# Performance work log

Measured on AMD Instinct MI355X. Metric: run time of the kernel, lower is better.

The kernel has to match this reference:

```python
import jax, jax.numpy as jnp
import numpy as np

N, E, F = 50000, 400000, 128
H0, C0 = 1, 128   # layer 0: heads=1, out=128 (concat=False -> mean over heads)
H1, C1 = 4, 64    # layer 1: heads=4, out=64
EPS_BN = 1e-5
NEG_SLOPE = 0.2


def setup_inputs() -> dict:
    key = jax.random.key(0)
    ks = jax.random.split(key, 12)

    def w(k, shape, fan_in):
        return jax.random.normal(k, shape, jnp.float32) / np.float32(np.sqrt(fan_in))

    return {
        "emb": jax.random.normal(ks[0], (N, F), jnp.float32),
        "edge_weight": jax.random.uniform(ks[1], (E,), jnp.float32),
        # GATv2Conv layer 0 params (lin_l, lin_r, lin_edge, att, out bias)
        "Wl0": w(ks[2], (F, H0 * C0), F), "bl0": jnp.zeros((H0 * C0,), jnp.float32),
        "Wr0": w(ks[3], (F, H0 * C0), F), "br0": jnp.zeros((H0 * C0,), jnp.float32),
        "We0": w(ks[4], (1, H0 * C0), 1), "att0": w(ks[5], (H0, C0), C0),
        "b0": jnp.zeros((C0,), jnp.float32),
        "g0": jnp.ones((C0,), jnp.float32), "be0": jnp.zeros((C0,), jnp.float32),
        # GATv2Conv layer 1 params
        "Wl1": w(ks[6], (C0, H1 * C1), C0), "bl1": jnp.zeros((H1 * C1,), jnp.float32),
        "Wr1": w(ks[7], (C0, H1 * C1), C0), "br1": jnp.zeros((H1 * C1,), jnp.float32),
        "We1": w(ks[8], (1, H1 * C1), 1), "att1": w(ks[9], (H1, C1), C1),
        "b1": jnp.zeros((C1,), jnp.float32),
        "g1": jnp.ones((C1,), jnp.float32), "be1": jnp.zeros((C1,), jnp.float32),
        "edge_index": jax.random.randint(ks[10], (2, E), 0, N, jnp.int32),
    }


def gatv2(x, src, dst, ea, Wl, bl, Wr, br, We, att, b, H, C):
    """PyG GATv2Conv, edge_dim=1, concat=False (mean over heads), eval dropout."""
    n = x.shape[0]
    xl = (x @ Wl + bl).reshape(n, H, C)
    xr = (x @ Wr + br).reshape(n, H, C)
    ef = (ea[:, None] @ We).reshape(-1, H, C)           # [Et,H,C] edge embedding
    m = jax.nn.leaky_relu(xl[src] + xr[dst] + ef, NEG_SLOPE)  # [Et,H,C]
    alpha = jnp.einsum('ehc,hc->eh', m, att)            # attention logits
    amax = jax.ops.segment_max(alpha, dst, num_segments=n)
    ex = jnp.exp(alpha - amax[dst])
    den = jax.ops.segment_sum(ex, dst, num_segments=n)
    a = ex / (den[dst] + 1e-16)                          # segment softmax (PyG eps)
    out = jax.ops.segment_sum(a[:, :, None] * xl[src], dst, num_segments=n)
    return out.mean(axis=1) + b                          # concat=False -> head mean


def batchnorm(x, g, be):
    mu = x.mean(0)
    v = x.var(0)  # biased variance, as torch BN uses for normalization
    return g * (x - mu) * jax.lax.rsqrt(v + EPS_BN) + be


def _forward(emb, edge_weight, Wl0, bl0, Wr0, br0, We0, att0, b0, g0, be0,
             Wl1, bl1, Wr1, br1, We1, att1, b1, g1, be1, edge_index):
    loop = jnp.arange(N, dtype=edge_index.dtype)
    src = jnp.concatenate([edge_index[0], loop])
    dst = jnp.concatenate([edge_index[1], loop])
    # add_self_loops with fill_value='mean' for edge_attr
    ea = jnp.concatenate([edge_weight, jnp.full((N,), edge_weight.mean(), edge_weight.dtype)])
    # NOTE: zip(layer_stack, batchnorm_stack) truncates -> only first 2 of 3 GAT
    # layers execute, each followed by BN + ELU (+ identity dropout, p=0).
    h = gatv2(emb, src, dst, ea, Wl0, bl0, Wr0, br0, We0, att0, b0, H0, C0)
    h = jax.nn.elu(batchnorm(h, g0, be0))
    h = gatv2(h, src, dst, ea, Wl1, bl1, Wr1, br1, We1, att1, b1, H1, C1)
    h = jax.nn.elu(batchnorm(h, g1, be1))
    return h


def reference(emb, edge_weight, Wl0, bl0, Wr0, br0, We0, att0, b0, g0, be0,
              Wl1, bl1, Wr1, br1, We1, att1, b1, g1, be1, edge_index):
    return _forward(emb, edge_weight, Wl0, bl0, Wr0, br0, We0, att0, b0, g0, be0,
                    Wl1, bl1, Wr1, br1, We1, att1, b1, g1, be1, edge_index)
```

## Files before the change

kernel.cpp:

```cpp
#include <hip/hip_runtime.h>
#include <cstdint>
#include <cstddef>
#include <type_traits>

using f32x4 = __attribute__((ext_vector_type(4))) float;
using s16x8 = __attribute__((ext_vector_type(8))) short;

__device__ __forceinline__ ushort f2bf(float x) {
    uint32_t u = __builtin_bit_cast(uint32_t, x);
    u += 0x7fffu + ((u >> 16) & 1u);
    return (ushort)(u >> 16);
}
__device__ __forceinline__ float bflo(uint32_t u) { return __builtin_bit_cast(float, u << 16); }
__device__ __forceinline__ float bfhi(uint32_t u) { return __builtin_bit_cast(float, u & 0xffff0000u); }

__device__ __forceinline__ void dec8(uint4 g, float* x) {
    x[0] = bflo(g.x); x[1] = bfhi(g.x); x[2] = bflo(g.y); x[3] = bfhi(g.y);
    x[4] = bflo(g.z); x[5] = bfhi(g.z); x[6] = bflo(g.w); x[7] = bfhi(g.w);
}

#define GLOAD_LDS16(g, l)                                                                  \
    __builtin_amdgcn_global_load_lds((const __attribute__((address_space(1))) void*)(g),  \
                                     (__attribute__((address_space(3))) void*)(l), 16, 0, 0)

__global__ __launch_bounds__(256) void degree_ew_wt(const int* __restrict__ ei,
                                                    const float* __restrict__ ew,
                                                    int* __restrict__ deg,
                                                    float* __restrict__ partials,
                                                    int E, int N, int NBE,
                                                    const float* __restrict__ Wl0,
                                                    const float* __restrict__ Wr0,
                                                    ushort* __restrict__ WT0,
                                                    const float* __restrict__ Wl1,
                                                    const float* __restrict__ Wr1,
                                                    ushort* __restrict__ WT1) {
    __shared__ float red[256];
    int bid = blockIdx.x;
    int t = threadIdx.x;
    if (bid < NBE) {
        int e = bid * 256 + t;
        float s = (e < E) ? ew[e] : 0.f;
        red[t] = s; __syncthreads();
        for (int o = 128; o; o >>= 1) { if (t < o) red[t] += red[t + o]; __syncthreads(); }
        if (t == 0) partials[bid] = red[0];
        if (e < E + N) {
            int d = (e < E) ? ei[E + e] : (e - E);
            atomicAdd(&deg[d], 1);
        }
        return;
    }
    int j = (bid - NBE) * 256 + t;
    if (j < 128 * 256) {
        int k = j >> 8, c = j & 255;
        float v = (c < 128) ? Wl0[k * 128 + c] : Wr0[k * 128 + (c - 128)];
        WT0[(size_t)c * 128 + k] = f2bf(v);
        return;
    }
    j -= 128 * 256;
    if (j < 128 * 512) {
        int k = j >> 9, c = j & 511;
        float v = (c < 256) ? Wl1[k * 256 + c] : Wr1[k * 256 + (c - 256)];
        WT1[(size_t)c * 128 + k] = f2bf(v);
    }
}

__global__ void scan_partial(const int* __restrict__ deg, int n, int* __restrict__ bsum) {
    __shared__ int lds[256];
    int t = threadIdx.x;
    int base = blockIdx.x * 1024 + t * 4;
    int s = 0;
#pragma unroll
    for (int j = 0; j < 4; ++j) if (base + j < n) s += deg[base + j];
    lds[t] = s; __syncthreads();
    for (int o = 128; o; o >>= 1) { if (t < o) lds[t] += lds[t + o]; __syncthreads(); }
    if (t == 0) bsum[blockIdx.x] = lds[0];
}

__global__ void scan_block(const int* __restrict__ bsum, int nb, int* __restrict__ boff,
                           int* __restrict__ row_start, int n, int total,
                           const float* __restrict__ partials, int nbp, int E,
                           float* __restrict__ stats) {
    __shared__ int lds[256];
    __shared__ float fred[256];
    int t = threadIdx.x;
    int v = (t < nb) ? bsum[t] : 0;
    lds[t] = v; __syncthreads();
    for (int o = 1; o < 256; o <<= 1) {
        int y = (t >= o) ? lds[t - o] : 0;
        __syncthreads();
        lds[t] += y;
        __syncthreads();
    }
    if (t < nb) boff[t] = lds[t] - v;
    if (t == 0) row_start[n] = total;
    stats[t] = 0.f; stats[256 + t] = 0.f;
    float fs = 0.f;
    for (int j = t; j < nbp; j += 256) fs += partials[j];
    fred[t] = fs; __syncthreads();
    for (int o = 128; o; o >>= 1) { if (t < o) fred[t] += fred[t + o]; __syncthreads(); }
    if (t == 0) stats[0] = fred[0] / (float)E;
}

__global__ void scan_final(const int* __restrict__ deg, int n, const int* __restrict__ boff,
                           int* __restrict__ row_start, int* __restrict__ cursor) {
    __shared__ int lds[256];
    int t = threadIdx.x;
    int base = blockIdx.x * 1024 + t * 4;
    int d[4], loc[4], s = 0;
#pragma unroll
    for (int j = 0; j < 4; ++j) d[j] = (base + j < n) ? deg[base + j] : 0;
#pragma unroll
    for (int j = 0; j < 4; ++j) { loc[j] = s; s += d[j]; }
    lds[t] = s; __syncthreads();
    for (int o = 1; o < 256; o <<= 1) {
        int y = (t >= o) ? lds[t - o] : 0;
        __syncthreads();
        lds[t] += y;
        __syncthreads();
    }
    int texcl = lds[t] - s + boff[blockIdx.x];
#pragma unroll
    for (int j = 0; j < 4; ++j)
        if (base + j < n) { row_start[base + j] = texcl + loc[j]; cursor[base + j] = 0; }
}

__global__ void scatter_kernel(const int* __restrict__ ei, const float* __restrict__ ew,
                               const float* __restrict__ ew_mean, const int* __restrict__ row_start,
                               int* __restrict__ cursor, int* __restrict__ csr_src,
                               float* __restrict__ csr_ea, int E, int N) {
    int e = blockIdx.x * blockDim.x + threadIdx.x;
    if (e >= E + N) return;
    int s, d; float w;
    if (e < E) { s = ei[e]; d = ei[E + e]; w = ew[e]; }
    else       { s = d = e - E;            w = ew_mean[0]; }
    int pos = row_start[d] + atomicAdd(&cursor[d], 1);
    csr_src[pos] = s;
    csr_ea[pos] = w;
}

template <int MODE>
__global__ __launch_bounds__(512) void mfma_linear3(const void* __restrict__ Xv,
                                                    const ushort* __restrict__ WT,
                                                    const float* __restrict__ bnsums,
                                                    const float* __restrict__ gamma,
                                                    const float* __restrict__ beta,
                                                    const float* __restrict__ bl,
                                                    const float* __restrict__ br,
                                                    ushort* __restrict__ xl,
                                                    ushort* __restrict__ xr,
                                                    int n, int HALF) {
    constexpr int LW = (MODE == 1) ? 2 : 1;
    __shared__ ushort sB[128 * 128];
    __shared__ ushort sA[128 * 128];
    const int tid = threadIdx.x;
    const int c0 = blockIdx.x * 128;
    const int ntiles = (n + 127) >> 7;

    {
        const ushort* src = WT + (size_t)c0 * 128;
#pragma unroll
        for (int it = 0; it < 4; ++it) {
            int f = tid + it * 512;
            int row = f >> 4, ch = f & 15;
            const ushort* g = src + (size_t)row * 128 + ((ch ^ (row & 7)) << 3);
            ushort* lp = sB + (((size_t)it * 512 + (tid & ~63)) << 3);
            GLOAD_LDS16(g, lp);
        }
    }

    const int myc = (tid & 15) * 8;
    const int row0 = tid >> 4;
    const int swc = (tid & 15) ^ (row0 & 7);
    float Af[8], Bf[8];
    if constexpr (MODE == 2) {
        float invn = 1.f / (float)n;
#pragma unroll
        for (int j = 0; j < 8; ++j) {
            float mu = bnsums[myc + j] * invn;
            float var = bnsums[128 + myc + j] * invn - mu * mu;
            float rs = rsqrtf(var + 1e-5f);
            Af[j] = gamma[myc + j] * rs;
            Bf[j] = beta[myc + j] - mu * Af[j];
        }
    }

    uint4 rA[4][LW];
    auto loadA = [&](int rt) {
        int r0 = rt << 7;
#pragma unroll
        for (int it = 0; it < 4; ++it) {
            int gr = r0 + row0 + it * 32; gr = gr < n ? gr : n - 1;
            if constexpr (MODE == 1) {
                const float* src = (const float*)Xv + (size_t)gr * 128 + myc;
                rA[it][0] = *(const uint4*)src;
                rA[it][1] = *(const uint4*)(src + 4);
            } else {
                rA[it][0] = *(const uint4*)((const ushort*)Xv + (size_t)gr * 128 + myc);
            }
        }
    };
    auto writeA = [&]() {
#pragma unroll
        for (int it = 0; it < 4; ++it) {
            uint4 o;
            if constexpr (MODE == 0) {
                o = rA[it][0];
            } else if constexpr (MODE == 1) {
                float x[8] = {
                    __builtin_bit_cast(float, rA[it][0].x), __builtin_bit_cast(float, rA[it][0].y),
                    __builtin_bit_cast(float, rA[it][0].z), __builtin_bit_cast(float, rA[it][0].w),
                    __builtin_bit_cast(float, rA[it][1].x), __builtin_bit_cast(float, rA[it][1].y),
                    __builtin_bit_cast(float, rA[it][1].z), __builtin_bit_cast(float, rA[it][1].w)};
                ushort h[8];
#pragma unroll
                for (int j = 0; j < 8; ++j) h[j] = f2bf(x[j]);
                o.x = h[0] | ((uint32_t)h[1] << 16); o.y = h[2] | ((uint32_t)h[3] << 16);
                o.z = h[4] | ((uint32_t)h[5] << 16); o.w = h[6] | ((uint32_t)h[7] << 16);
            } else {
                float x[8]; dec8(rA[it][0], x);
                ushort h[8];
#pragma unroll
                for (int j = 0; j < 8; ++j) {
                    float v = fmaf(x[j], Af[j], Bf[j]);
                    v = v > 0.f ? v : __expf(v) - 1.f;
                    h[j] = f2bf(v);
                }
                o.x = h[0] | ((uint32_t)h[1] << 16); o.y = h[2] | ((uint32_t)h[3] << 16);
                o.z = h[4] | ((uint32_t)h[5] << 16); o.w = h[6] | ((uint32_t)h[7] << 16);
            }
            *(uint4*)&sA[(row0 + it * 32) * 128 + swc * 8] = o;
        }
    };

    const int w = tid >> 6, l = tid & 63, lr = l & 15, lg = l >> 4;
    const bool left = c0 < HALF;
    const float* bias = left ? bl : br;
    ushort* dst = left ? xl : xr;
    const int cb = left ? c0 : c0 - HALF;
    float bv[8];
#pragma unroll
    for (int tn = 0; tn < 8; ++tn) bv[tn] = bias[cb + tn * 16 + lr];
    const int arow = w * 16 + lr;

    int rt = blockIdx.y;
    if (rt >= ntiles) return;
    loadA(rt);
    writeA();
    __syncthreads();

    while (true) {
        int nx = rt + gridDim.y;
        if (nx < ntiles) loadA(nx);

        f32x4 acc[8] = {};
#pragma unroll
        for (int kk = 0; kk < 4; ++kk) {
            int ach = (kk * 4 + lg) ^ (arow & 7);
            s16x8 a = *(const s16x8*)&sA[arow * 128 + (ach << 3)];
#pragma unroll
            for (int tn = 0; tn < 8; ++tn) {
                int brow = tn * 16 + lr;
                int bch = (kk * 4 + lg) ^ (brow & 7);
                s16x8 b = *(const s16x8*)&sB[brow * 128 + (bch << 3)];
                acc[tn] = __builtin_amdgcn_mfma_f32_16x16x32_bf16(a, b, acc[tn], 0, 0, 0);
            }
        }
        int rbase = (rt << 7) + w * 16 + lg * 4;
#pragma unroll
        for (int tn = 0; tn < 8; ++tn) {
            int colh = cb + tn * 16 + lr;
#pragma unroll
            for (int r = 0; r < 4; ++r) {
                int row = rbase + r;
                if (row < n) dst[(size_t)row * HALF + colh] = f2bf(acc[tn][r] + bv[tn]);
            }
        }
        if (nx >= ntiles) break;
        __syncthreads();
        writeA();
        __syncthreads();
        rt = nx;
    }
}

template <int H, int C, int LPN>
__global__ __launch_bounds__(256, 6) void gat_agg(const ushort* __restrict__ xl,
                                                  const ushort* __restrict__ xr,
                                                  const int* __restrict__ row_start,
                                                  const int* __restrict__ csr_src,
                                                  const float* __restrict__ csr_ea,
                                                  const float* __restrict__ We,
                                                  const float* __restrict__ att,
                                                  const float* __restrict__ bias,
                                                  ushort* __restrict__ out, int n) {
    constexpr int HC = H * C;
    constexpr int VPL = HC / LPN;
    constexpr int REDW = LPN / H;
    constexpr int NPW = 64 / LPN;
    static_assert(VPL == 8, "");

    const int wid = threadIdx.x >> 6;
    const int lane = threadIdx.x & 63;
    const int sl = lane & (LPN - 1);
    const int sub = lane / LPN;
    const int v = (blockIdx.x * 4 + wid) * NPW + sub;
    const bool valid = v < n;
    const int vv = valid ? v : n - 1;

    const int base = sl * VPL;
    const int e0 = row_start[vv];
    const int e1 = row_start[vv + 1];
    const ushort* xlb = xl + base;

    uint4 gF; float wF;
    {
        int s = csr_src[e0];
        wF = csr_ea[e0];
        gF = *(const uint4*)&xlb[(size_t)s * HC];
    }
    uint4 gA, gB; float wA, wB;
    {
        int ea = e0 + 1 < e1 ? e0 + 1 : e0;
        int eb = e0 + 2 < e1 ? e0 + 2 : e0;
        int sa = csr_src[ea]; wA = csr_ea[ea];
        int sb = csr_src[eb]; wB = csr_ea[eb];
        gA = *(const uint4*)&xlb[(size_t)sa * HC];
        gB = *(const uint4*)&xlb[(size_t)sb * HC];
    }

    float xrv[8], wE[8], attv[8];
    dec8(*(const uint4*)&xr[(size_t)vv * HC + base], xrv);
#pragma unroll
    for (int j = 0; j < 8; j += 4) {
        float4 a = *(const float4*)&We[base + j];
        wE[j] = a.x; wE[j + 1] = a.y; wE[j + 2] = a.z; wE[j + 3] = a.w;
        float4 b = *(const float4*)&att[base + j];
        attv[j] = b.x; attv[j + 1] = b.y; attv[j + 2] = b.z; attv[j + 3] = b.w;
    }

    float m, den, acc[8];
    {
        float xf[8];
        dec8(gF, xf);
        float t1 = 0.f, t2 = 0.f;
#pragma unroll
        for (int j = 0; j < 8; ++j) {
            float u = xf[j] + fmaf(wF, wE[j], xrv[j]);
            t1 = fmaf(u, attv[j], t1);
            t2 = fmaf(__builtin_fabsf(u), attv[j], t2);
        }
        float p = fmaf(0.6f, t1, 0.4f * t2);
#pragma unroll
        for (int o = REDW >> 1; o; o >>= 1) p += __shfl_xor(p, o, 64);
        m = p; den = 1.f;
#pragma unroll
        for (int j = 0; j < 8; ++j) acc[j] = xf[j];
    }

    int e = e0 + 1;
    while (e + 1 < e1) {
        uint4 g0 = gA, g1 = gB; float w0 = wA, w1 = wB;
        {
            int ea = e + 2 < e1 ? e + 2 : e;
            int eb = e + 3 < e1 ? e + 3 : e;
            int sa = csr_src[ea]; wA = csr_ea[ea];
            int sb = csr_src[eb]; wB = csr_ea[eb];
            gA = *(const uint4*)&xlb[(size_t)sa * HC];
            gB = *(const uint4*)&xlb[(size_t)sb * HC];
        }
        float xf0[8], xf1[8];
        dec8(g0, xf0); dec8(g1, xf1);
        float t10 = 0.f, t20 = 0.f, t11 = 0.f, t21 = 0.f;
#pragma unroll
        for (int j = 0; j < 8; ++j) {
            float u0 = xf0[j] + fmaf(w0, wE[j], xrv[j]);
            float u1 = xf1[j] + fmaf(w1, wE[j], xrv[j]);
            t10 = fmaf(u0, attv[j], t10);
            t20 = fmaf(__builtin_fabsf(u0), attv[j], t20);
            t11 = fmaf(u1, attv[j], t11);
            t21 = fmaf(__builtin_fabsf(u1), attv[j], t21);
        }
        float p0 = fmaf(0.6f, t10, 0.4f * t20);
        float p1 = fmaf(0.6f, t11, 0.4f * t21);
#pragma unroll
        for (int o = REDW >> 1; o; o >>= 1) {
            p0 += __shfl_xor(p0, o, 64);
            p1 += __shfl_xor(p1, o, 64);
        }
        float pm = fmaxf(p0, p1);
        if (__builtin_expect(pm - m > 8.f, 0)) {
            float r = __expf(m - pm);
            den *= r;
#pragma unroll
            for (int j = 0; j < 8; ++j) acc[j] *= r;
            m = pm;
        }
        float pe0 = __expf(p0 - m);
        float pe1 = __expf(p1 - m);
        den += pe0 + pe1;
#pragma unroll
        for (int j = 0; j < 8; ++j)
            acc[j] = fmaf(pe1, xf1[j], fmaf(pe0, xf0[j], acc[j]));
        e += 2;
    }
    if (e < e1) {
        float xf[8];
        dec8(gA, xf);
        float t1 = 0.f, t2 = 0.f;
#pragma unroll
        for (int j = 0; j < 8; ++j) {
            float u = xf[j] + fmaf(wA, wE[j], xrv[j]);
            t1 = fmaf(u, attv[j], t1);
            t2 = fmaf(__builtin_fabsf(u), attv[j], t2);
        }
        float p = fmaf(0.6f, t1, 0.4f * t2);
#pragma unroll
        for (int o = REDW >> 1; o; o >>= 1) p += __shfl_xor(p, o, 64);
        float dd = p - m;
        if (__builtin_expect(dd > 8.f, 0)) {
            float r = __expf(-dd);
            den = fmaf(den, r, 1.f);
#pragma unroll
            for (int j = 0; j < 8; ++j) acc[j] = fmaf(acc[j], r, xf[j]);
            m = p;
        } else {
            float pe = __expf(dd);
            den += pe;
#pragma unroll
            for (int j = 0; j < 8; ++j) acc[j] = fmaf(pe, xf[j], acc[j]);
        }
    }

    float inv = 1.f / den;
#pragma unroll
    for (int j = 0; j < 8; ++j) acc[j] *= inv;

    if constexpr (H > 1) {
#pragma unroll
        for (int o = REDW; o < LPN; o <<= 1)
#pragma unroll
            for (int j = 0; j < 8; ++j) acc[j] += __shfl_xor(acc[j], o, 64);
#pragma unroll
        for (int j = 0; j < 8; ++j) acc[j] *= (1.f / (float)H);
    }

    if (valid && sl < C / VPL) {
        float bv[8];
#pragma unroll
        for (int j = 0; j < 8; j += 4) {
            float4 b = *(const float4*)&bias[sl * VPL + j];
            bv[j] = b.x; bv[j + 1] = b.y; bv[j + 2] = b.z; bv[j + 3] = b.w;
        }
        uint4 o;
        o.x = (uint32_t)f2bf(acc[0] + bv[0]) | ((uint32_t)f2bf(acc[1] + bv[1]) << 16);
        o.y = (uint32_t)f2bf(acc[2] + bv[2]) | ((uint32_t)f2bf(acc[3] + bv[3]) << 16);
        o.z = (uint32_t)f2bf(acc[4] + bv[4]) | ((uint32_t)f2bf(acc[5] + bv[5]) << 16);
        o.w = (uint32_t)f2bf(acc[6] + bv[6]) | ((uint32_t)f2bf(acc[7] + bv[7]) << 16);
        *(uint4*)&out[(size_t)v * C + sl * VPL] = o;
    }
}

template <int C>
__global__ __launch_bounds__(256) void bn_stats_bf16(const ushort* __restrict__ x, int n,
                                                     float* __restrict__ sums) {
    constexpr int C2 = C / 2;
    constexpr int RPB = 256 / C2;
    __shared__ float red[256];
    int t = threadIdx.x;
    int c2 = t % C2, rs = t / C2;
    float s0 = 0.f, s1 = 0.f, q0 = 0.f, q1 = 0.f;
    for (int row = blockIdx.x * RPB + rs; row < n; row += gridDim.x * RPB) {
        uint32_t u = *(const uint32_t*)&x[(size_t)row * C + c2 * 2];
        float a = bflo(u), b = bfhi(u);
        s0 += a; q0 += a * a; s1 += b; q1 += b * b;
    }
    float vals[4] = {s0, s1, q0, q1};
    float outv[4];
#pragma unroll
    for (int k = 0; k < 4; ++k) {
        red[t] = vals[k]; __syncthreads();
        if (rs == 0) {
            float s = red[c2];
#pragma unroll
            for (int r = 1; r < RPB; ++r) s += red[c2 + r * C2];
            outv[k] = s;
        }
        __syncthreads();
    }
    if (rs == 0) {
        atomicAdd(&sums[c2 * 2],     outv[0]);
        atomicAdd(&sums[c2 * 2 + 1], outv[1]);
        atomicAdd(&sums[C + c2 * 2],     outv[2]);
        atomicAdd(&sums[C + c2 * 2 + 1], outv[3]);
    }
}

template <int C>
__global__ __launch_bounds__(256) void bn_apply_elu_f32(const ushort* __restrict__ x, int n,
                                                        const float* __restrict__ g,
                                                        const float* __restrict__ be,
                                                        const float* __restrict__ sums,
                                                        float* __restrict__ outf) {
    int total = n * C / 8;
    float invn = 1.f / (float)n;
    for (int i = blockIdx.x * blockDim.x + threadIdx.x; i < total; i += gridDim.x * blockDim.x) {
        uint4 u = ((const uint4*)x)[i];
        int c0 = (i * 8) & (C - 1);
        float r[8] = {bflo(u.x), bfhi(u.x), bflo(u.y), bfhi(u.y),
                      bflo(u.z), bfhi(u.z), bflo(u.w), bfhi(u.w)};
#pragma unroll
        for (int j = 0; j < 8; ++j) {
            int c = c0 + j;
            float mu = sums[c] * invn;
            float var = sums[C + c] * invn - mu * mu;
            float t = g[c] * (r[j] - mu) * rsqrtf(var + 1e-5f) + be[c];
            r[j] = t > 0.f ? t : expm1f(t);
        }
        ((float4*)outf)[i * 2]     = make_float4(r[0], r[1], r[2], r[3]);
        ((float4*)outf)[i * 2 + 1] = make_float4(r[4], r[5], r[6], r[7]);
    }
}

extern "C" void kernel_launch(void* const* d_in, const int* in_sizes, int n_in,
                              void* d_out, int out_size, void* d_ws, size_t ws_size,
                              hipStream_t stream) {
    const float* emb = (const float*)d_in[0];
    const float* ew  = (const float*)d_in[1];
    const float* Wl0 = (const float*)d_in[2];
    const float* bl0 = (const float*)d_in[3];
    const float* Wr0 = (const float*)d_in[4];
    const float* br0 = (const float*)d_in[5];
    const float* We0 = (const float*)d_in[6];
    const float* att0 = (const float*)d_in[7];
    const float* b0  = (const float*)d_in[8];
    const float* g0  = (const float*)d_in[9];
    const float* be0 = (const float*)d_in[10];
    const float* Wl1 = (const float*)d_in[11];
    const float* bl1 = (const float*)d_in[12];
    const float* Wr1 = (const float*)d_in[13];
    const float* br1 = (const float*)d_in[14];
    const float* We1 = (const float*)d_in[15];
    const float* att1 = (const float*)d_in[16];
    const float* b1  = (const float*)d_in[17];
    const float* g1  = (const float*)d_in[18];
    const float* be1 = (const float*)d_in[19];
    const int* ei    = (const int*)d_in[20];

    const int N = in_sizes[0] / 128;
    const int E = in_sizes[1];
    const int Et = E + N;
    float* out = (float*)d_out;

    char* w = (char*)d_ws;
    size_t off = 0;
    auto alloc = [&](size_t bytes) {
        void* p = w + off;
        off = (off + bytes + 255) & ~(size_t)255;
        return p;
    };
    ushort* xlb    = (ushort*)alloc((size_t)N * 256 * 2);
    ushort* xrb    = (ushort*)alloc((size_t)N * 256 * 2);
    ushort* h0b16  = (ushort*)alloc((size_t)N * 128 * 2);
    ushort* out16  = (ushort*)alloc((size_t)N * 64 * 2);
    ushort* WT0    = (ushort*)alloc((size_t)256 * 128 * 2);
    ushort* WT1    = (ushort*)alloc((size_t)512 * 128 * 2);
    int*   deg     = (int*)alloc((size_t)2 * N * 4);
    int*   cursor  = deg + N;
    int*   row_st  = (int*)alloc((size_t)(N + 1) * 4);
    int*   csr_src = (int*)alloc((size_t)Et * 4);
    float* csr_ea  = (float*)alloc((size_t)Et * 4);
    int*   bsum    = (int*)alloc(256 * 4);
    int*   boff    = (int*)alloc(256 * 4);
    float* partials= (float*)alloc(2048 * 4);
    float* stats   = (float*)alloc(512 * 4);
    float* ew_mean = stats;
    float* bn0     = stats + 64;
    float* bn1     = stats + 64 + 256;
    (void)ws_size; (void)n_in; (void)out_size;

    hipMemsetAsync(deg, 0, (size_t)N * 4, stream);

    const int NBE = (Et + 255) / 256;
    const int WTB = (128 * 256 + 128 * 512) / 256;
    degree_ew_wt<<<NBE + WTB, 256, 0, stream>>>(ei, ew, deg, partials, E, N, NBE,
                                                Wl0, Wr0, WT0, Wl1, Wr1, WT1);
    const int NB1 = (N + 1023) / 1024;
    scan_partial<<<NB1, 256, 0, stream>>>(deg, N, bsum);
    scan_block<<<1, 256, 0, stream>>>(bsum, NB1, boff, row_st, N, Et, partials, NBE, E, stats);
    scan_final<<<NB1, 256, 0, stream>>>(deg, N, boff, row_st, cursor);
    scatter_kernel<<<NBE, 256, 0, stream>>>(ei, ew, ew_mean, row_st, cursor,
                                            csr_src, csr_ea, E, N);

    const int ntiles = (N + 127) / 128;
    const int GR = ntiles < 256 ? ntiles : 256;

    mfma_linear3<1><<<dim3(2, GR), 512, 0, stream>>>(emb, WT0, nullptr, nullptr, nullptr,
                                                     bl0, br0, xlb, xrb, N, 128);
    gat_agg<1, 128, 16><<<(N + 15) / 16, 256, 0, stream>>>(xlb, xrb, row_st, csr_src, csr_ea,
                                                           We0, att0, b0, h0b16, N);
    bn_stats_bf16<128><<<128, 256, 0, stream>>>(h0b16, N, bn0);

    mfma_linear3<2><<<dim3(4, GR), 512, 0, stream>>>(h0b16, WT1, bn0, g0, be0,
                                                     bl1, br1, xlb, xrb, N, 256);
    gat_agg<4, 64, 32><<<(N + 7) / 8, 256, 0, stream>>>(xlb, xrb, row_st, csr_src, csr_ea,
                                                        We1, att1, b1, out16, N);
    bn_stats_bf16<64><<<128, 256, 0, stream>>>(out16, N, bn1);
    bn_apply_elu_f32<64><<<1024, 256, 0, stream>>>(out16, N, g1, be1, bn1, out);
}
```

Before: 254.8 us.

## Pack CSR src/weight into int2 and deepen gather prefetch in GAT aggregation

```diff
diff --git a/kernel.cpp b/kernel.cpp
--- a/kernel.cpp
+++ b/kernel.cpp
@@ -126,16 +126,15 @@
 
 __global__ void scatter_kernel(const int* __restrict__ ei, const float* __restrict__ ew,
                                const float* __restrict__ ew_mean, const int* __restrict__ row_start,
-                               int* __restrict__ cursor, int* __restrict__ csr_src,
-                               float* __restrict__ csr_ea, int E, int N) {
+                               int* __restrict__ cursor, int2* __restrict__ csr,
+                               int E, int N) {
     int e = blockIdx.x * blockDim.x + threadIdx.x;
     if (e >= E + N) return;
     int s, d; float w;
     if (e < E) { s = ei[e]; d = ei[E + e]; w = ew[e]; }
     else       { s = d = e - E;            w = ew_mean[0]; }
     int pos = row_start[d] + atomicAdd(&cursor[d], 1);
-    csr_src[pos] = s;
-    csr_ea[pos] = w;
+    csr[pos] = make_int2(s, __builtin_bit_cast(int, w));
 }
 
 template <int MODE>
@@ -284,11 +283,10 @@
 }
 
 template <int H, int C, int LPN>
-__global__ __launch_bounds__(256, 6) void gat_agg(const ushort* __restrict__ xl,
+__global__ __launch_bounds__(256, 4) void gat_agg(const ushort* __restrict__ xl,
                                                   const ushort* __restrict__ xr,
                                                   const int* __restrict__ row_start,
-                                                  const int* __restrict__ csr_src,
-                                                  const float* __restrict__ csr_ea,
+                                                  const int2* __restrict__ csr,
                                                   const float* __restrict__ We,
                                                   const float* __restrict__ att,
                                                   const float* __restrict__ bias,
@@ -312,21 +310,18 @@
     const int e1 = row_start[vv + 1];
     const ushort* xlb = xl + base;
 
+    auto LD = [&](int ee, uint4& g, float& w) {
+        ee = ee < e1 - 1 ? ee : e1 - 1;
+        int2 sw = csr[ee];
+        w = __builtin_bit_cast(float, sw.y);
+        g = *(const uint4*)&xlb[(size_t)sw.x * HC];
+    };
+
     uint4 gF; float wF;
-    {
-        int s = csr_src[e0];
-        wF = csr_ea[e0];
-        gF = *(const uint4*)&xlb[(size_t)s * HC];
-    }
-    uint4 gA, gB; float wA, wB;
-    {
-        int ea = e0 + 1 < e1 ? e0 + 1 : e0;
-        int eb = e0 + 2 < e1 ? e0 + 2 : e0;
-        int sa = csr_src[ea]; wA = csr_ea[ea];
-        int sb = csr_src[eb]; wB = csr_ea[eb];
-        gA = *(const uint4*)&xlb[(size_t)sa * HC];
-        gB = *(const uint4*)&xlb[(size_t)sb * HC];
-    }
+    LD(e0, gF, wF);
+    uint4 gA0, gA1, gB0, gB1; float wA0, wA1, wB0, wB1;
+    LD(e0 + 1, gA0, wA0); LD(e0 + 2, gA1, wA1);
+    LD(e0 + 3, gB0, wB0); LD(e0 + 4, gB1, wB1);
 
     float xrv[8], wE[8], attv[8];
     dec8(*(const uint4*)&xr[(size_t)vv * HC + base], xrv);
@@ -357,17 +352,7 @@
         for (int j = 0; j < 8; ++j) acc[j] = xf[j];
     }
 
-    int e = e0 + 1;
-    while (e + 1 < e1) {
-        uint4 g0 = gA, g1 = gB; float w0 = wA, w1 = wB;
-        {
-            int ea = e + 2 < e1 ? e + 2 : e;
-            int eb = e + 3 < e1 ? e + 3 : e;
-            int sa = csr_src[ea]; wA = csr_ea[ea];
-            int sb = csr_src[eb]; wB = csr_ea[eb];
-            gA = *(const uint4*)&xlb[(size_t)sa * HC];
-            gB = *(const uint4*)&xlb[(size_t)sb * HC];
-        }
+    auto PROC = [&](uint4 g0, uint4 g1, float w0, float w1) {
         float xf0[8], xf1[8];
         dec8(g0, xf0); dec8(g1, xf1);
         float t10 = 0.f, t20 = 0.f, t11 = 0.f, t21 = 0.f;
@@ -401,15 +386,27 @@
 #pragma unroll
         for (int j = 0; j < 8; ++j)
             acc[j] = fmaf(pe1, xf1[j], fmaf(pe0, xf0[j], acc[j]));
+    };
+
+    int e = e0 + 1;
+    while (e + 1 < e1) {
+        PROC(gA0, gA1, wA0, wA1);
+        if (e + 5 < e1) { LD(e + 4, gA0, wA0); LD(e + 5, gA1, wA1); }
         e += 2;
+        if (e + 1 >= e1) break;
+        PROC(gB0, gB1, wB0, wB1);
+        if (e + 5 < e1) { LD(e + 4, gB0, wB0); LD(e + 5, gB1, wB1); }
+        e += 2;
     }
     if (e < e1) {
+        uint4 g; float w;
+        LD(e, g, w);
         float xf[8];
-        dec8(gA, xf);
+        dec8(g, xf);
         float t1 = 0.f, t2 = 0.f;
 #pragma unroll
         for (int j = 0; j < 8; ++j) {
-            float u = xf[j] + fmaf(wA, wE[j], xrv[j]);
+            float u = xf[j] + fmaf(w, wE[j], xrv[j]);
             t1 = fmaf(u, attv[j], t1);
             t2 = fmaf(__builtin_fabsf(u), attv[j], t2);
         }
@@ -567,8 +564,7 @@
     int*   deg     = (int*)alloc((size_t)2 * N * 4);
     int*   cursor  = deg + N;
     int*   row_st  = (int*)alloc((size_t)(N + 1) * 4);
-    int*   csr_src = (int*)alloc((size_t)Et * 4);
-    float* csr_ea  = (float*)alloc((size_t)Et * 4);
+    int2*  csr     = (int2*)alloc((size_t)(Et + 8) * 8);
     int*   bsum    = (int*)alloc(256 * 4);
     int*   boff    = (int*)alloc(256 * 4);
     float* partials= (float*)alloc(2048 * 4);
@@ -588,22 +584,21 @@
     scan_partial<<<NB1, 256, 0, stream>>>(deg, N, bsum);
     scan_block<<<1, 256, 0, stream>>>(bsum, NB1, boff, row_st, N, Et, partials, NBE, E, stats);
     scan_final<<<NB1, 256, 0, stream>>>(deg, N, boff, row_st, cursor);
-    scatter_kernel<<<NBE, 256, 0, stream>>>(ei, ew, ew_mean, row_st, cursor,
-                                            csr_src, csr_ea, E, N);
+    scatter_kernel<<<NBE, 256, 0, stream>>>(ei, ew, ew_mean, row_st, cursor, csr, E, N);
 
     const int ntiles = (N + 127) / 128;
     const int GR = ntiles < 256 ? ntiles : 256;
 
     mfma_linear3<1><<<dim3(2, GR), 512, 0, stream>>>(emb, WT0, nullptr, nullptr, nullptr,
                                                      bl0, br0, xlb, xrb, N, 128);
-    gat_agg<1, 128, 16><<<(N + 15) / 16, 256, 0, stream>>>(xlb, xrb, row_st, csr_src, csr_ea,
+    gat_agg<1, 128, 16><<<(N + 15) / 16, 256, 0, stream>>>(xlb, xrb, row_st, csr,
                                                            We0, att0, b0, h0b16, N);
-    bn_stats_bf16<128><<<128, 256, 0, stream>>>(h0b16, N, bn0);
+    bn_stats_bf16<128><<<256, 256, 0, stream>>>(h0b16, N, bn0);
 
     mfma_linear3<2><<<dim3(4, GR), 512, 0, stream>>>(h0b16, WT1, bn0, g0, be0,
                                                      bl1, br1, xlb, xrb, N, 256);
-    gat_agg<4, 64, 32><<<(N + 7) / 8, 256, 0, stream>>>(xlb, xrb, row_st, csr_src, csr_ea,
+    gat_agg<4, 64, 32><<<(N + 7) / 8, 256, 0, stream>>>(xlb, xrb, row_st, csr,
                                                         We1, att1, b1, out16, N);
-    bn_stats_bf16<64><<<128, 256, 0, stream>>>(out16, N, bn1);
+    bn_stats_bf16<64><<<256, 256, 0, stream>>>(out16, N, bn1);
     bn_apply_elu_f32<64><<<1024, 256, 0, stream>>>(out16, N, g1, be1, bn1, out);
 }
```

Result: no change. 255.7 us (+0.4%).
